# Kernel tuning notes

Measured on AMD Instinct MI355X. Metric: run time of the kernel, lower is better.

The kernel has to match this reference:

```python
import jax, jax.numpy as jnp
import numpy as np

N = 8388608          # number of samples (2**23)
T_MAX = 100000       # number of distinct time values -> ~84 ties per time


def setup_inputs() -> dict:
    key = jax.random.key(0)
    k1, k2, k3 = jax.random.split(key, 3)
    inp = jax.random.normal(k1, (N,), dtype=jnp.float32)            # log hazards
    target = jax.random.randint(k2, (N,), 0, T_MAX, dtype=jnp.int32)  # times
    weight = jax.random.randint(k3, (N,), 0, 2, dtype=jnp.int32)      # event indicator
    return {"input": inp, "target": target, "weight": weight}


def _cox_efron_npll(log_hz, time, event):
    """Negative Cox partial log-likelihood with Efron tie correction, mean reduction.

    Faithful to torchsurv's _partial_likelihood_efron: per unique time j,
    pll_j = sum_{i in H_j} log_hz_i - sum_{l=0}^{m_j-1} log(D_j - (l/m_j)*T_j)
    where H_j = events at time j, D_j = sum of exp(log_hz) over risk set (t>=t_j),
    T_j = sum of exp(log_hz) over H_j, m_j = |H_j|; loss = -mean over j with m_j>0.
    """
    n = log_hz.shape[0]
    order = jnp.argsort(time)                       # sort by time (group-sum math is tie-order invariant)
    t = time[order]
    lh = log_hz[order]
    ev = event[order].astype(lh.dtype)

    # group id per sample: 0..(num_unique-1), padded groups beyond that are empty
    new_grp = jnp.concatenate([jnp.zeros((1,), jnp.int32), (t[1:] != t[:-1]).astype(jnp.int32)])
    seg = jnp.cumsum(new_grp)                       # [n] int32

    hz = jnp.exp(lh)
    grp_hz = jax.ops.segment_sum(hz, seg, num_segments=n)          # sum exp per time group
    denom_naive = jnp.cumsum(grp_hz[::-1])[::-1]                   # risk-set sums (suffix over groups)
    m = jax.ops.segment_sum(ev, seg, num_segments=n)               # events per group
    log_nom = jax.ops.segment_sum(lh * ev, seg, num_segments=n)    # sum of log_hz over H_j
    ties = jax.ops.segment_sum(hz * ev, seg, num_segments=n)       # sum of exp over H_j

    # rank l in [0, m_j) of each event within its group
    csum_e = jnp.cumsum(ev)
    events_before = jnp.concatenate([jnp.zeros((1,), lh.dtype), jnp.cumsum(m)[:-1]])
    rank = csum_e - 1.0 - events_before[seg]
    mg = jnp.maximum(m[seg], 1.0)
    term = jnp.where(ev > 0.0,
                     jnp.log(denom_naive[seg] - (rank / mg) * ties[seg]),
                     0.0)
    log_denom = jax.ops.segment_sum(term, seg, num_segments=n)

    include = (m > 0.0).astype(lh.dtype)
    pll = jnp.where(m > 0.0, log_nom - log_denom, 0.0)
    # reduction='mean': -pll.nanmean() over groups that contain events
    return -(jnp.sum(pll) / jnp.sum(include))


def reference(input, target, weight):
    return _cox_efron_npll(input, target, weight)
```

## Files before the change

kernel.cpp:

```cpp
#include <hip/hip_runtime.h>

#define TMAXV 100000
#define CHUNK 256
#define NCHUNK ((TMAXV + CHUNK - 1) / CHUNK)
#define WB 256
#define LOGWB 8
#define SB ((TMAXV + WB - 1) / WB)
#define TILE 4096
#define RPT 16
#define KS 8
#define CAP 4096
#define RPH (CAP / 256)


__device__ __forceinline__ float block_reduce_sum(float v, float* sdata) {
    int lane = threadIdx.x & 63;
    int wid  = threadIdx.x >> 6;
    #pragma unroll
    for (int off = 32; off > 0; off >>= 1)
        v += __shfl_down(v, off, 64);
    if (lane == 0) sdata[wid] = v;
    __syncthreads();
    if (wid == 0) {
        v = (lane < 4) ? sdata[lane] : 0.0f;
        v += __shfl_down(v, 2, 64);
        v += __shfl_down(v, 1, 64);
    }
    return v;
}


__global__ void count_kernel(const int* __restrict__ tgt,
                             int* __restrict__ blkcnt, int n, int nt) {
    __shared__ int lc[SB];
    for (int i = threadIdx.x; i < SB; i += blockDim.x) lc[i] = 0;
    __syncthreads();
    int tile = blockIdx.x;
    int lo = tile * TILE;
    int hi = min(n, lo + TILE);
    for (int i = lo + threadIdx.x; i < hi; i += blockDim.x)
        atomicAdd(&lc[tgt[i] >> LOGWB], 1);
    __syncthreads();
    for (int s = threadIdx.x; s < SB; s += blockDim.x)
        blkcnt[s * nt + tile] = lc[s];
}

__global__ void tile_scan_kernel(const int* __restrict__ blkcnt,
                                 int* __restrict__ tilebase,
                                 int* __restrict__ totals, int nt) {
    __shared__ int ls[256];
    int s   = blockIdx.x;
    int tid = threadIdx.x;
    int run = 0;
    for (int t0 = 0; t0 < nt; t0 += 256) {
        int t = t0 + tid;
        int c = (t < nt) ? blkcnt[s * nt + t] : 0;
        ls[tid] = c;
        __syncthreads();
        for (int off = 1; off < 256; off <<= 1) {
            int a = (tid >= off) ? ls[tid - off] : 0;
            __syncthreads();
            ls[tid] += a;
            __syncthreads();
        }
        int incl = ls[tid];
        int tot  = ls[255];
        if (t < nt) tilebase[s * nt + t] = run + incl - c;
        run += tot;
        __syncthreads();
    }
    if (tid == 0) totals[s] = run;
}

__global__ void bucket_base_kernel(const int* __restrict__ totals,
                                   int* __restrict__ base, int n) {
    __shared__ int ls[512];
    int tid = threadIdx.x;
    int c = (tid < SB) ? totals[tid] : 0;
    ls[tid] = c;
    __syncthreads();
    for (int off = 1; off < 512; off <<= 1) {
        int a = (tid >= off) ? ls[tid - off] : 0;
        __syncthreads();
        ls[tid] += a;
        __syncthreads();
    }
    if (tid < SB) base[tid] = ls[tid] - c;
    if (tid == 0) base[SB] = n;
}

__global__ void scatter_kernel(const float* __restrict__ lh,
                               const int*   __restrict__ tgt,
                               const int*   __restrict__ ev,
                               const int*   __restrict__ blkcnt,
                               const int*   __restrict__ tilebase,
                               const int*   __restrict__ base,
                               unsigned* __restrict__ val,
                               double* __restrict__ acc, int n, int nt) {
    __shared__ unsigned fu[TILE];
    __shared__ int pfx[SB];
    __shared__ int lrank[SB];
    __shared__ int tb[SB];
    __shared__ int ls[512];
    __shared__ float sdata[4];
    int tid  = threadIdx.x;
    int tile = blockIdx.x;
    int lo   = tile * TILE;
    int cnt_here = min(TILE, n - lo);

    int c0   = (tid < SB)  ? blkcnt[tid  * nt + tile] : 0;
    int idx1 = tid + 256;
    int c1   = (idx1 < SB) ? blkcnt[idx1 * nt + tile] : 0;
    for (int s = tid; s < SB; s += 256) {
        lrank[s] = 0;
        tb[s]    = base[s] + tilebase[s * nt + tile];
    }
    ls[tid]  = c0;
    ls[idx1] = c1;
    __syncthreads();
    for (int off = 1; off < 512; off <<= 1) {
        int a0 = (tid  >= off) ? ls[tid  - off] : 0;
        int a1 = (idx1 >= off) ? ls[idx1 - off] : 0;
        __syncthreads();
        ls[tid]  += a0;
        ls[idx1] += a1;
        __syncthreads();
    }
    if (tid  < SB) pfx[tid]  = ls[tid]  - c0;
    if (idx1 < SB) pfx[idx1] = ls[idx1] - c1;

    unsigned rb[RPT];
    int      rk[RPT];
    float xl = 0.f;
    #pragma unroll
    for (int k = 0; k < RPT; ++k) {
        int i = lo + k * 256 + tid;
        if (i < n) {
            int t = tgt[i];
            int e = ev[i] & 1;
            float x = lh[i];
            float h = __expf(x);
            unsigned bits = (__float_as_uint(h) & 0x7FFFFF00u)
                          | (unsigned)(t & (WB - 1))
                          | ((unsigned)e << 31);
            rb[k] = bits;
            rk[k] = t >> LOGWB;
            if (e) xl += x;
        } else {
            rk[k] = -1;
        }
    }
    __syncthreads();

    #pragma unroll
    for (int k = 0; k < RPT; ++k) {
        if (rk[k] >= 0) {
            int r = atomicAdd(&lrank[rk[k]], 1);
            fu[pfx[rk[k]] + r] = rb[k];
        }
    }
    __syncthreads();

    for (int p = tid; p < cnt_here; p += 256) {
        int loB = 0, hiB = SB;
        #pragma unroll
        for (int it = 0; it < 9; ++it) {
            int mid = (loB + hiB) >> 1;
            if (pfx[mid] <= p) loB = mid; else hiB = mid;
        }
        val[tb[loB] + (p - pfx[loB])] = fu[p];
    }

    float rl = block_reduce_sum(xl, sdata);
    if (tid == 0) atomicAdd(&acc[2], (double)rl);
}

__global__ void bucket_hist_kernel(const unsigned* __restrict__ val,
                                   const int* __restrict__ base,
                                   float* __restrict__ partials) {
    __shared__ unsigned fv[CAP];
    __shared__ unsigned cnt[WB];
    __shared__ unsigned rankc[WB];
    __shared__ unsigned pfx[WB];
    __shared__ unsigned ls[WB];
    int tid = threadIdx.x;
    int b   = blockIdx.x >> 3;
    int k   = blockIdx.x & (KS - 1);
    int lo0 = base[b], len = base[b + 1] - lo0;
    int lo  = lo0 + (int)(((long long)len * k) / KS);
    int hi  = lo0 + (int)(((long long)len * (k + 1)) / KS);

    float sh = 0.f, cm = 0.f, th = 0.f;

    for (int c0 = lo; c0 < hi; c0 += CAP) {
        int c1 = min(hi, c0 + CAP);
        cnt[tid] = 0; rankc[tid] = 0;
        __syncthreads();

        unsigned rv[RPH];
        int      rs[RPH];
        #pragma unroll
        for (int u = 0; u < RPH; ++u) {
            int i = c0 + u * 256 + tid;
            if (i < c1) {
                rv[u] = val[i];
                rs[u] = (int)(rv[u] & (WB - 1));
                atomicAdd(&cnt[rs[u]], 1u);
            } else {
                rs[u] = -1;
            }
        }
        __syncthreads();

        unsigned c = cnt[tid];
        ls[tid] = c;
        __syncthreads();
        for (int off = 1; off < 256; off <<= 1) {
            unsigned a = (tid >= off) ? ls[tid - off] : 0u;
            __syncthreads();
            ls[tid] += a;
            __syncthreads();
        }
        pfx[tid] = ls[tid] - c;
        __syncthreads();

        #pragma unroll
        for (int u = 0; u < RPH; ++u) {
            if (rs[u] >= 0) {
                unsigned r = atomicAdd(&rankc[rs[u]], 1u);
                fv[pfx[rs[u]] + r] = rv[u];
            }
        }
        __syncthreads();

        int s0 = (int)pfx[tid], e0 = s0 + (int)cnt[tid];
        for (int p = s0; p < e0; ++p) {
            unsigned bits = fv[p];
            float h = fabsf(__uint_as_float(bits));
            sh += h;
            if (bits >> 31) { cm += 1.0f; th += h; }
        }
        __syncthreads();
    }

    float* pbase = partials + (size_t)blockIdx.x * 3 * WB;
    pbase[0 * WB + tid] = sh;
    pbase[1 * WB + tid] = cm;
    pbase[2 * WB + tid] = th;
}

__global__ void merge_kernel(const float* __restrict__ partials,
                             float* __restrict__ sum_hz,
                             float* __restrict__ mcnt,
                             float* __restrict__ ties,
                             float* __restrict__ chunk_sum) {
    __shared__ float sdata[4];
    int tid = threadIdx.x;
    int b   = blockIdx.x;
    float sh = 0.f, cm = 0.f, th = 0.f;
    #pragma unroll
    for (int k = 0; k < KS; ++k) {
        const float* pbase = partials + (size_t)(b * KS + k) * 3 * WB;
        sh += pbase[0 * WB + tid];
        cm += pbase[1 * WB + tid];
        th += pbase[2 * WB + tid];
    }
    int t = (b << LOGWB) + tid;
    float shv = (t < TMAXV) ? sh : 0.f;
    if (t < TMAXV) {
        sum_hz[t] = sh;
        mcnt[t]   = cm;
        ties[t]   = th;
    }
    float cs = block_reduce_sum(shv, sdata);
    if (tid == 0) chunk_sum[b] = cs;
}

__global__ void chunk_scan_kernel(const float* __restrict__ chunk_sum,
                                  double* __restrict__ chunk_off) {
    __shared__ double ds[512];
    int tid = threadIdx.x;
    double own = (tid < NCHUNK) ? (double)chunk_sum[tid] : 0.0;
    ds[tid] = own;
    __syncthreads();
    for (int off = 1; off < 512; off <<= 1) {
        double add = (tid + off < 512) ? ds[tid + off] : 0.0;
        __syncthreads();
        ds[tid] += add;
        __syncthreads();
    }
    if (tid < NCHUNK) chunk_off[tid] = ds[tid] - own;
}

__global__ void pll_suffix_kernel(const float* __restrict__ sum_hz,
                                  const float* __restrict__ mcnt,
                                  const float* __restrict__ ties,
                                  const double* __restrict__ chunk_off,
                                  double* __restrict__ acc) {
    __shared__ float sf[CHUNK];
    __shared__ float sdata[4];
    __shared__ float sdata2[4];
    int tid = threadIdx.x;
    int t   = blockIdx.x * CHUNK + tid;
    float v = (t < TMAXV) ? sum_hz[t] : 0.0f;
    sf[tid] = v;
    __syncthreads();
    for (int off = 1; off < CHUNK; off <<= 1) {
        float add = (tid + off < CHUNK) ? sf[tid + off] : 0.0f;
        __syncthreads();
        sf[tid] += add;
        __syncthreads();
    }
    float pll = 0.0f, inc = 0.0f;
    if (t < TMAXV) {
        float mv = mcnt[t];
        if (mv > 0.5f) {
            float D    = (float)(chunk_off[blockIdx.x] + (double)sf[tid]);
            float T    = ties[t];
            int   mi   = (int)(mv + 0.5f);
            float step = T / mv;
            float s = 0.0f;
            for (int l = 0; l < mi; ++l)
                s += __logf(D - (float)l * step);
            pll = -s;
            inc = 1.0f;
        }
    }
    float rp = block_reduce_sum(pll, sdata);
    __syncthreads();
    float ri = block_reduce_sum(inc, sdata2);
    if (threadIdx.x == 0) {
        atomicAdd(&acc[0], (double)rp);
        atomicAdd(&acc[1], (double)ri);
    }
}

__global__ void finalize_kernel(const double* __restrict__ acc,
                                float* __restrict__ out) {
    double cnt = acc[1];
    out[0] = (cnt > 0.0) ? (float)(-(acc[0] + acc[2]) / cnt) : 0.0f;
}

__global__ void hist_kernel(const float* __restrict__ lh,
                            const int*   __restrict__ tgt,
                            const int*   __restrict__ ev,
                            float* __restrict__ sum_hz,
                            float* __restrict__ mcnt,
                            float* __restrict__ log_nom,
                            float* __restrict__ ties,
                            int n) {
    int i = blockIdx.x * blockDim.x + threadIdx.x;
    if (i >= n) return;
    float x = lh[i];
    int   t = tgt[i];
    int   e = ev[i];
    float h = __expf(x);
    unsafeAtomicAdd(&sum_hz[t], h);
    if (e) {
        unsafeAtomicAdd(&mcnt[t], 1.0f);
        unsafeAtomicAdd(&log_nom[t], x);
        unsafeAtomicAdd(&ties[t], h);
    }
}

__global__ void chunk_sum_kernel(const float* __restrict__ sum_hz,
                                 float* __restrict__ chunk_sum) {
    __shared__ float sdata[4];
    int i = blockIdx.x * CHUNK + threadIdx.x;
    float v = (i < TMAXV) ? sum_hz[i] : 0.0f;
    v = block_reduce_sum(v, sdata);
    if (threadIdx.x == 0) chunk_sum[blockIdx.x] = v;
}

__global__ void pll_kernel(const float* __restrict__ mcnt,
                           const float* __restrict__ log_nom,
                           const float* __restrict__ ties,
                           const float* __restrict__ sum_hz,
                           const double* __restrict__ chunk_off,
                           double* __restrict__ acc) {
    __shared__ float sf[CHUNK];
    __shared__ float sdata[4];
    __shared__ float sdata2[4];
    int tid = threadIdx.x;
    int t   = blockIdx.x * CHUNK + tid;
    float v = (t < TMAXV) ? sum_hz[t] : 0.0f;
    sf[tid] = v;
    __syncthreads();
    for (int off = 1; off < CHUNK; off <<= 1) {
        float add = (tid + off < CHUNK) ? sf[tid + off] : 0.0f;
        __syncthreads();
        sf[tid] += add;
        __syncthreads();
    }
    float pll = 0.0f, inc = 0.0f;
    if (t < TMAXV) {
        float mv = mcnt[t];
        if (mv > 0.5f) {
            float D    = (float)(chunk_off[blockIdx.x] + (double)sf[tid]);
            float T    = ties[t];
            int   mi   = (int)(mv + 0.5f);
            float step = T / mv;
            float s = 0.0f;
            for (int l = 0; l < mi; ++l)
                s += __logf(D - (float)l * step);
            pll = log_nom[t] - s;
            inc = 1.0f;
        }
    }
    float rp = block_reduce_sum(pll, sdata);
    __syncthreads();
    float ri = block_reduce_sum(inc, sdata2);
    if (threadIdx.x == 0) {
        atomicAdd(&acc[0], (double)rp);
        atomicAdd(&acc[1], (double)ri);
    }
}

extern "C" void kernel_launch(void* const* d_in, const int* in_sizes, int n_in,
                              void* d_out, int out_size, void* d_ws, size_t ws_size,
                              hipStream_t stream) {
    const float* lh  = (const float*)d_in[0];
    const int*   tgt = (const int*)d_in[1];
    const int*   ev  = (const int*)d_in[2];
    float*       out = (float*)d_out;
    int n  = in_sizes[0];
    int nt = (n + TILE - 1) / TILE;

    char* ws = (char*)d_ws;
    size_t off = 0;
    auto take = [&](size_t bytes, size_t align) {
        off = (off + align - 1) & ~(align - 1);
        size_t r = off; off += bytes; return r;
    };
    size_t o_acc    = take(32, 16);
    size_t o_sum    = take((size_t)TMAXV * 4, 16);
    size_t o_m      = take((size_t)TMAXV * 4, 16);
    size_t o_ties   = take((size_t)TMAXV * 4, 16);
    size_t o_base   = take((size_t)(SB + 1) * 4, 4);
    size_t o_totals = take((size_t)SB * 4, 4);
    size_t o_csum   = take((size_t)NCHUNK * 4, 16);
    size_t o_coff   = take((size_t)NCHUNK * 8, 8);
    size_t o_blkcnt = take((size_t)nt * SB * 4, 16);
    size_t o_tbase  = take((size_t)nt * SB * 4, 16);
    size_t o_val    = take((size_t)n * 4, 16);
    size_t o_part   = take((size_t)SB * KS * 3 * WB * 4, 16);
    size_t need     = off;

    if (ws_size >= need) {
        double*   acc      = (double*)(ws + o_acc);
        float*    sum_hz   = (float*)(ws + o_sum);
        float*    mcnt     = (float*)(ws + o_m);
        float*    ties     = (float*)(ws + o_ties);
        int*      base     = (int*)(ws + o_base);
        int*      totals   = (int*)(ws + o_totals);
        float*    chunk_sum= (float*)(ws + o_csum);
        double*   chunk_off= (double*)(ws + o_coff);
        int*      blkcnt   = (int*)(ws + o_blkcnt);
        int*      tilebase = (int*)(ws + o_tbase);
        unsigned* val      = (unsigned*)(ws + o_val);
        float*    partials = (float*)(ws + o_part);

        hipMemsetAsync(d_ws, 0, 32, stream);

        count_kernel<<<nt, 256, 0, stream>>>(tgt, blkcnt, n, nt);
        tile_scan_kernel<<<SB, 256, 0, stream>>>(blkcnt, tilebase, totals, nt);
        bucket_base_kernel<<<1, 512, 0, stream>>>(totals, base, n);
        scatter_kernel<<<nt, 256, 0, stream>>>(lh, tgt, ev, blkcnt, tilebase, base, val, acc, n, nt);
        bucket_hist_kernel<<<SB * KS, 256, 0, stream>>>(val, base, partials);
        merge_kernel<<<SB, 256, 0, stream>>>(partials, sum_hz, mcnt, ties, chunk_sum);
        chunk_scan_kernel<<<1, 512, 0, stream>>>(chunk_sum, chunk_off);
        pll_suffix_kernel<<<NCHUNK, 256, 0, stream>>>(sum_hz, mcnt, ties, chunk_off, acc);
        finalize_kernel<<<1, 1, 0, stream>>>(acc, out);
    } else {
        size_t f = 0;
        auto ftake = [&](size_t bytes, size_t align) {
            f = (f + align - 1) & ~(align - 1);
            size_t r = f; f += bytes; return r;
        };
        size_t f_acc  = ftake(32, 16);
        size_t f_sum  = ftake((size_t)TMAXV * 4, 16);
        size_t f_m    = ftake((size_t)TMAXV * 4, 16);
        size_t f_ln   = ftake((size_t)TMAXV * 4, 16);
        size_t f_ties = ftake((size_t)TMAXV * 4, 16);
        size_t zb     = f;
        size_t f_csum = ftake((size_t)NCHUNK * 4, 16);
        size_t f_coff = ftake((size_t)NCHUNK * 8, 8);

        double* acc     = (double*)(ws + f_acc);
        float*  sum_hz  = (float*)(ws + f_sum);
        float*  mcnt    = (float*)(ws + f_m);
        float*  log_nom = (float*)(ws + f_ln);
        float*  ties    = (float*)(ws + f_ties);
        float*  chunk_sum = (float*)(ws + f_csum);
        double* chunk_off = (double*)(ws + f_coff);

        hipMemsetAsync(d_ws, 0, zb, stream);

        hist_kernel<<<(n + 255) / 256, 256, 0, stream>>>(lh, tgt, ev, sum_hz, mcnt, log_nom, ties, n);
        chunk_sum_kernel<<<NCHUNK, 256, 0, stream>>>(sum_hz, chunk_sum);
        chunk_scan_kernel<<<1, 512, 0, stream>>>(chunk_sum, chunk_off);
        pll_kernel<<<NCHUNK, 256, 0, stream>>>(mcnt, log_nom, ties, sum_hz, chunk_off, acc);
        finalize_kernel<<<1, 1, 0, stream>>>(acc, out);
    }
}
```

Baseline: 242.9 us.

## Move per-tile prefix into count pass, transpose counts, fold merge into hist/suffix

```diff
diff --git a/kernel.cpp b/kernel.cpp
--- a/kernel.cpp
+++ b/kernel.cpp
@@ -6,6 +6,7 @@
 #define WB 256
 #define LOGWB 8
 #define SB ((TMAXV + WB - 1) / WB)
+#define SBP 512
 #define TILE 4096
 #define RPT 16
 #define KS 8
@@ -30,31 +31,60 @@
 }
 
 
-__global__ void count_kernel(const int* __restrict__ tgt,
-                             int* __restrict__ blkcnt, int n, int nt) {
-    __shared__ int lc[SB];
-    for (int i = threadIdx.x; i < SB; i += blockDim.x) lc[i] = 0;
-    __syncthreads();
-    int tile = blockIdx.x;
-    int lo = tile * TILE;
-    int hi = min(n, lo + TILE);
-    for (int i = lo + threadIdx.x; i < hi; i += blockDim.x)
+__global__ void count_pfx_kernel(const int* __restrict__ tgt,
+                                 int* __restrict__ pfx_arr,
+                                 int* __restrict__ cnt_t, int n) {
+    __shared__ int lc[SBP];
+    __shared__ int ls[SBP];
+    int tid = threadIdx.x, tile = blockIdx.x;
+    lc[tid] = 0; lc[tid + 256] = 0;
+    __syncthreads();
+    int lo = tile * TILE, hi = min(n, lo + TILE);
+    for (int i = lo + tid; i < hi; i += 256)
         atomicAdd(&lc[tgt[i] >> LOGWB], 1);
     __syncthreads();
-    for (int s = threadIdx.x; s < SB; s += blockDim.x)
-        blkcnt[s * nt + tile] = lc[s];
-}
-
-__global__ void tile_scan_kernel(const int* __restrict__ blkcnt,
-                                 int* __restrict__ tilebase,
+    int c0 = lc[tid], c1 = lc[tid + 256];
+    int i1 = tid + 256;
+    ls[tid] = c0; ls[i1] = c1;
+    __syncthreads();
+    for (int off = 1; off < SBP; off <<= 1) {
+        int a0 = (tid >= off) ? ls[tid - off] : 0;
+        int a1 = (i1  >= off) ? ls[i1  - off] : 0;
+        __syncthreads();
+        ls[tid] += a0; ls[i1] += a1;
+        __syncthreads();
+    }
+    size_t rb = (size_t)tile * SBP;
+    pfx_arr[rb + tid] = ls[tid] - c0;
+    pfx_arr[rb + i1]  = ls[i1]  - c1;
+    cnt_t[rb + tid] = c0;
+    cnt_t[rb + i1]  = c1;
+}
+
+__global__ void transpose_kernel(const int* __restrict__ A,
+                                 int* __restrict__ B, int rows, int cols) {
+    __shared__ int tl[32][33];
+    int bx = blockIdx.x * 32, by = blockIdx.y * 32;
+    int x = threadIdx.x, y = threadIdx.y;
+    #pragma unroll
+    for (int j = 0; j < 32; j += 8)
+        if (by + y + j < rows && bx + x < cols)
+            tl[y + j][x] = A[(size_t)(by + y + j) * cols + bx + x];
+    __syncthreads();
+    #pragma unroll
+    for (int j = 0; j < 32; j += 8)
+        if (bx + y + j < cols && by + x < rows)
+            B[(size_t)(bx + y + j) * rows + by + x] = tl[x][y + j];
+}
+
+__global__ void tile_scan_kernel(int* __restrict__ cnt_s,
                                  int* __restrict__ totals, int nt) {
     __shared__ int ls[256];
-    int s   = blockIdx.x;
-    int tid = threadIdx.x;
+    int s = blockIdx.x, tid = threadIdx.x;
     int run = 0;
     for (int t0 = 0; t0 < nt; t0 += 256) {
         int t = t0 + tid;
-        int c = (t < nt) ? blkcnt[s * nt + t] : 0;
+        int c = (t < nt) ? cnt_s[(size_t)s * nt + t] : 0;
         ls[tid] = c;
         __syncthreads();
         for (int off = 1; off < 256; off <<= 1) {
@@ -65,7 +95,7 @@
         }
         int incl = ls[tid];
         int tot  = ls[255];
-        if (t < nt) tilebase[s * nt + t] = run + incl - c;
+        if (t < nt) cnt_s[(size_t)s * nt + t] = run + incl - c;
         run += tot;
         __syncthreads();
     }
@@ -74,62 +104,48 @@
 
 __global__ void bucket_base_kernel(const int* __restrict__ totals,
                                    int* __restrict__ base, int n) {
-    __shared__ int ls[512];
+    __shared__ int ls[SBP];
     int tid = threadIdx.x;
-    int c = (tid < SB) ? totals[tid] : 0;
+    int c = totals[tid];
     ls[tid] = c;
     __syncthreads();
-    for (int off = 1; off < 512; off <<= 1) {
+    for (int off = 1; off < SBP; off <<= 1) {
         int a = (tid >= off) ? ls[tid - off] : 0;
         __syncthreads();
         ls[tid] += a;
         __syncthreads();
     }
-    if (tid < SB) base[tid] = ls[tid] - c;
-    if (tid == 0) base[SB] = n;
+    base[tid] = ls[tid] - c;
+    if (tid == 0) base[SBP] = n;
 }
 
 __global__ void scatter_kernel(const float* __restrict__ lh,
                                const int*   __restrict__ tgt,
                                const int*   __restrict__ ev,
-                               const int*   __restrict__ blkcnt,
-                               const int*   __restrict__ tilebase,
+                               const int*   __restrict__ pfx_arr,
+                               const int*   __restrict__ tilebase_t,
                                const int*   __restrict__ base,
                                unsigned* __restrict__ val,
-                               double* __restrict__ acc, int n, int nt) {
+                               double* __restrict__ acc, int n) {
     __shared__ unsigned fu[TILE];
-    __shared__ int pfx[SB];
-    __shared__ int lrank[SB];
-    __shared__ int tb[SB];
-    __shared__ int ls[512];
+    __shared__ int pfx[SBP];
+    __shared__ int tb[SBP];
+    __shared__ int lrank[SBP];
     __shared__ float sdata[4];
     int tid  = threadIdx.x;
     int tile = blockIdx.x;
     int lo   = tile * TILE;
     int cnt_here = min(TILE, n - lo);
-
-    int c0   = (tid < SB)  ? blkcnt[tid  * nt + tile] : 0;
-    int idx1 = tid + 256;
-    int c1   = (idx1 < SB) ? blkcnt[idx1 * nt + tile] : 0;
-    for (int s = tid; s < SB; s += 256) {
-        lrank[s] = 0;
-        tb[s]    = base[s] + tilebase[s * nt + tile];
-    }
-    ls[tid]  = c0;
-    ls[idx1] = c1;
-    __syncthreads();
-    for (int off = 1; off < 512; off <<= 1) {
-        int a0 = (tid  >= off) ? ls[tid  - off] : 0;
-        int a1 = (idx1 >= off) ? ls[idx1 - off] : 0;
-        __syncthreads();
-        ls[tid]  += a0;
-        ls[idx1] += a1;
-        __syncthreads();
-    }
-    if (tid  < SB) pfx[tid]  = ls[tid]  - c0;
-    if (idx1 < SB) pfx[idx1] = ls[idx1] - c1;
-
-    unsigned rb[RPT];
+    int i1 = tid + 256;
+    size_t rb = (size_t)tile * SBP;
+
+    pfx[tid] = pfx_arr[rb + tid];
+    pfx[i1]  = pfx_arr[rb + i1];
+    tb[tid]  = base[tid] + tilebase_t[rb + tid];
+    tb[i1]   = base[i1]  + tilebase_t[rb + i1];
+    lrank[tid] = 0; lrank[i1] = 0;
+
+    unsigned rbits[RPT];
     int      rk[RPT];
     float xl = 0.f;
     #pragma unroll
@@ -140,10 +156,9 @@
             int e = ev[i] & 1;
             float x = lh[i];
             float h = __expf(x);
-            unsigned bits = (__float_as_uint(h) & 0x7FFFFF00u)
-                          | (unsigned)(t & (WB - 1))
-                          | ((unsigned)e << 31);
-            rb[k] = bits;
+            rbits[k] = (__float_as_uint(h) & 0x7FFFFF00u)
+                     | (unsigned)(t & (WB - 1))
+                     | ((unsigned)e << 31);
             rk[k] = t >> LOGWB;
             if (e) xl += x;
         } else {
@@ -156,13 +171,13 @@
     for (int k = 0; k < RPT; ++k) {
         if (rk[k] >= 0) {
             int r = atomicAdd(&lrank[rk[k]], 1);
-            fu[pfx[rk[k]] + r] = rb[k];
+            fu[pfx[rk[k]] + r] = rbits[k];
         }
     }
     __syncthreads();
 
     for (int p = tid; p < cnt_here; p += 256) {
-        int loB = 0, hiB = SB;
+        int loB = 0, hiB = SBP;
         #pragma unroll
         for (int it = 0; it < 9; ++it) {
             int mid = (loB + hiB) >> 1;
@@ -177,12 +192,14 @@
 
 __global__ void bucket_hist_kernel(const unsigned* __restrict__ val,
                                    const int* __restrict__ base,
-                                   float* __restrict__ partials) {
+                                   float* __restrict__ partials,
+                                   float* __restrict__ chunk_sum) {
     __shared__ unsigned fv[CAP];
     __shared__ unsigned cnt[WB];
     __shared__ unsigned rankc[WB];
     __shared__ unsigned pfx[WB];
     __shared__ unsigned ls[WB];
+    __shared__ float sdata[4];
     int tid = threadIdx.x;
     int b   = blockIdx.x >> 3;
     int k   = blockIdx.x & (KS - 1);
@@ -247,14 +264,33 @@
     pbase[0 * WB + tid] = sh;
     pbase[1 * WB + tid] = cm;
     pbase[2 * WB + tid] = th;
-}
-
-__global__ void merge_kernel(const float* __restrict__ partials,
-                             float* __restrict__ sum_hz,
-                             float* __restrict__ mcnt,
-                             float* __restrict__ ties,
-                             float* __restrict__ chunk_sum) {
+
+    float st = block_reduce_sum(sh, sdata);
+    if (tid == 0) unsafeAtomicAdd(&chunk_sum[b], st);
+}
+
+__global__ void chunk_scan_kernel(const float* __restrict__ chunk_sum,
+                                  double* __restrict__ chunk_off) {
+    __shared__ double ds[512];
+    int tid = threadIdx.x;
+    double own = (tid < NCHUNK) ? (double)chunk_sum[tid] : 0.0;
+    ds[tid] = own;
+    __syncthreads();
+    for (int off = 1; off < 512; off <<= 1) {
+        double add = (tid + off < 512) ? ds[tid + off] : 0.0;
+        __syncthreads();
+        ds[tid] += add;
+        __syncthreads();
+    }
+    if (tid < NCHUNK) chunk_off[tid] = ds[tid] - own;
+}
+
+__global__ void pll_suffix_kernel(const float* __restrict__ partials,
+                                  const double* __restrict__ chunk_off,
+                                  double* __restrict__ acc) {
+    __shared__ float sf[CHUNK];
     __shared__ float sdata[4];
+    __shared__ float sdata2[4];
     int tid = threadIdx.x;
     int b   = blockIdx.x;
     float sh = 0.f, cm = 0.f, th = 0.f;
@@ -265,45 +301,7 @@
         cm += pbase[1 * WB + tid];
         th += pbase[2 * WB + tid];
     }
-    int t = (b << LOGWB) + tid;
-    float shv = (t < TMAXV) ? sh : 0.f;
-    if (t < TMAXV) {
-        sum_hz[t] = sh;
-        mcnt[t]   = cm;
-        ties[t]   = th;
-    }
-    float cs = block_reduce_sum(shv, sdata);
-    if (tid == 0) chunk_sum[b] = cs;
-}
-
-__global__ void chunk_scan_kernel(const float* __restrict__ chunk_sum,
-                                  double* __restrict__ chunk_off) {
-    __shared__ double ds[512];
-    int tid = threadIdx.x;
-    double own = (tid < NCHUNK) ? (double)chunk_sum[tid] : 0.0;
-    ds[tid] = own;
-    __syncthreads();
-    for (int off = 1; off < 512; off <<= 1) {
-        double add = (tid + off < 512) ? ds[tid + off] : 0.0;
-        __syncthreads();
-        ds[tid] += add;
-        __syncthreads();
-    }
-    if (tid < NCHUNK) chunk_off[tid] = ds[tid] - own;
-}
-
-__global__ void pll_suffix_kernel(const float* __restrict__ sum_hz,
-                                  const float* __restrict__ mcnt,
-                                  const float* __restrict__ ties,
-                                  const double* __restrict__ chunk_off,
-                                  double* __restrict__ acc) {
-    __shared__ float sf[CHUNK];
-    __shared__ float sdata[4];
-    __shared__ float sdata2[4];
-    int tid = threadIdx.x;
-    int t   = blockIdx.x * CHUNK + tid;
-    float v = (t < TMAXV) ? sum_hz[t] : 0.0f;
-    sf[tid] = v;
+    sf[tid] = sh;
     __syncthreads();
     for (int off = 1; off < CHUNK; off <<= 1) {
         float add = (tid + off < CHUNK) ? sf[tid + off] : 0.0f;
@@ -311,20 +309,17 @@
         sf[tid] += add;
         __syncthreads();
     }
+    int t = b * CHUNK + tid;
     float pll = 0.0f, inc = 0.0f;
-    if (t < TMAXV) {
-        float mv = mcnt[t];
-        if (mv > 0.5f) {
-            float D    = (float)(chunk_off[blockIdx.x] + (double)sf[tid]);
-            float T    = ties[t];
-            int   mi   = (int)(mv + 0.5f);
-            float step = T / mv;
-            float s = 0.0f;
-            for (int l = 0; l < mi; ++l)
-                s += __logf(D - (float)l * step);
-            pll = -s;
-            inc = 1.0f;
-        }
+    if (t < TMAXV && cm > 0.5f) {
+        float D    = (float)(chunk_off[b] + (double)sf[tid]);
+        int   mi   = (int)(cm + 0.5f);
+        float step = th / cm;
+        float s = 0.0f;
+        for (int l = 0; l < mi; ++l)
+            s += __logf(D - (float)l * step);
+        pll = -s;
+        inc = 1.0f;
     }
     float rp = block_reduce_sum(pll, sdata);
     __syncthreads();
@@ -433,43 +428,45 @@
         size_t r = off; off += bytes; return r;
     };
     size_t o_acc    = take(32, 16);
-    size_t o_sum    = take((size_t)TMAXV * 4, 16);
-    size_t o_m      = take((size_t)TMAXV * 4, 16);
-    size_t o_ties   = take((size_t)TMAXV * 4, 16);
-    size_t o_base   = take((size_t)(SB + 1) * 4, 4);
-    size_t o_totals = take((size_t)SB * 4, 4);
-    size_t o_csum   = take((size_t)NCHUNK * 4, 16);
-    size_t o_coff   = take((size_t)NCHUNK * 8, 8);
-    size_t o_blkcnt = take((size_t)nt * SB * 4, 16);
-    size_t o_tbase  = take((size_t)nt * SB * 4, 16);
+    size_t o_csum   = take((size_t)SBP * 4, 16);
+    size_t zero_bytes = off;
+    size_t o_base   = take((size_t)(SBP + 1) * 4, 16);
+    size_t o_totals = take((size_t)SBP * 4, 16);
+    size_t o_coff   = take((size_t)NCHUNK * 8, 16);
+    size_t o_pfx    = take((size_t)nt * SBP * 4, 16);
+    size_t o_cntt   = take((size_t)nt * SBP * 4, 16);
+    size_t o_cnts   = take((size_t)nt * SBP * 4, 16);
     size_t o_val    = take((size_t)n * 4, 16);
-    size_t o_part   = take((size_t)SB * KS * 3 * WB * 4, 16);
     size_t need     = off;
+    size_t part_sz  = (size_t)SB * KS * 3 * WB * 4;
+    size_t o_part   = o_pfx;
+    if (o_part + part_sz > need) need = o_part + part_sz;
 
     if (ws_size >= need) {
-        double*   acc      = (double*)(ws + o_acc);
-        float*    sum_hz   = (float*)(ws + o_sum);
-        float*    mcnt     = (float*)(ws + o_m);
-        float*    ties     = (float*)(ws + o_ties);
-        int*      base     = (int*)(ws + o_base);
-        int*      totals   = (int*)(ws + o_totals);
-        float*    chunk_sum= (float*)(ws + o_csum);
-        double*   chunk_off= (double*)(ws + o_coff);
-        int*      blkcnt   = (int*)(ws + o_blkcnt);
-        int*      tilebase = (int*)(ws + o_tbase);
-        unsigned* val      = (unsigned*)(ws + o_val);
-        float*    partials = (float*)(ws + o_part);
-
-        hipMemsetAsync(d_ws, 0, 32, stream);
-
-        count_kernel<<<nt, 256, 0, stream>>>(tgt, blkcnt, n, nt);
-        tile_scan_kernel<<<SB, 256, 0, stream>>>(blkcnt, tilebase, totals, nt);
-        bucket_base_kernel<<<1, 512, 0, stream>>>(totals, base, n);
-        scatter_kernel<<<nt, 256, 0, stream>>>(lh, tgt, ev, blkcnt, tilebase, base, val, acc, n, nt);
-        bucket_hist_kernel<<<SB * KS, 256, 0, stream>>>(val, base, partials);
-        merge_kernel<<<SB, 256, 0, stream>>>(partials, sum_hz, mcnt, ties, chunk_sum);
+        double*   acc       = (double*)(ws + o_acc);
+        float*    chunk_sum = (float*)(ws + o_csum);
+        int*      base      = (int*)(ws + o_base);
+        int*      totals    = (int*)(ws + o_totals);
+        double*   chunk_off = (double*)(ws + o_coff);
+        int*      pfx_arr   = (int*)(ws + o_pfx);
+        int*      cnt_t     = (int*)(ws + o_cntt);
+        int*      cnt_s     = (int*)(ws + o_cnts);
+        unsigned* val       = (unsigned*)(ws + o_val);
+        float*    partials  = (float*)(ws + o_part);
+
+        hipMemsetAsync(d_ws, 0, zero_bytes, stream);
+
+        count_pfx_kernel<<<nt, 256, 0, stream>>>(tgt, pfx_arr, cnt_t, n);
+        transpose_kernel<<<dim3(SBP / 32, (nt + 31) / 32), dim3(32, 8), 0, stream>>>(
+            cnt_t, cnt_s, nt, SBP);
+        tile_scan_kernel<<<SBP, 256, 0, stream>>>(cnt_s, totals, nt);
+        bucket_base_kernel<<<1, SBP, 0, stream>>>(totals, base, n);
+        transpose_kernel<<<dim3((nt + 31) / 32, SBP / 32), dim3(32, 8), 0, stream>>>(
+            cnt_s, cnt_t, SBP, nt);
+        scatter_kernel<<<nt, 256, 0, stream>>>(lh, tgt, ev, pfx_arr, cnt_t, base, val, acc, n);
+        bucket_hist_kernel<<<SB * KS, 256, 0, stream>>>(val, base, partials, chunk_sum);
         chunk_scan_kernel<<<1, 512, 0, stream>>>(chunk_sum, chunk_off);
-        pll_suffix_kernel<<<NCHUNK, 256, 0, stream>>>(sum_hz, mcnt, ties, chunk_off, acc);
+        pll_suffix_kernel<<<NCHUNK, 256, 0, stream>>>(partials, chunk_off, acc);
         finalize_kernel<<<1, 1, 0, stream>>>(acc, out);
     } else {
         size_t f = 0;
```

Measured after the change: 243.0 us. No clear change (+0.1%).
